# Optimization experiments

Measured on AMD Instinct MI355X. Metric: run time of the kernel, lower is better.

The kernel has to match this reference:

```python
import jax, jax.numpy as jnp
import numpy as np

N, HID, MAXD, B, NCLS, GRUH = 50000, 128, 16, 50, 10, 32


def setup_inputs() -> dict:
    key = jax.random.key(0)
    ks = jax.random.split(key, 18)
    s = 0.05
    nrm = lambda k, shp: (jax.random.normal(k, shp, jnp.float32) * s)
    return {
        "feature": jax.random.normal(ks[0], (N, HID), jnp.float32),
        "nbr_idx": jax.random.randint(ks[1], (N, MAXD), 0, N, dtype=jnp.int32),
        "deg": jax.random.randint(ks[2], (N,), 1, MAXD + 1, dtype=jnp.int32),
        "graph_ids": (jnp.arange(N, dtype=jnp.int32) * B) // N,
        # SAGEConv(lstm) params: LSTM(in=HID, hidden=HID) + fc_self/fc_neigh
        "lstm_Wih": nrm(ks[3], (4 * HID, HID)),
        "lstm_Whh": nrm(ks[4], (4 * HID, HID)),
        "lstm_bih": nrm(ks[5], (4 * HID,)),
        "lstm_bhh": nrm(ks[6], (4 * HID,)),
        "W_self": nrm(ks[7], (HID, HID)),
        "W_neigh": nrm(ks[8], (HID, HID)),
        "b_sage": nrm(ks[9], (HID,)),
        # GraphConv params
        "W_gc": nrm(ks[10], (HID, HID)),
        "b_gc": nrm(ks[11], (HID,)),
        # GRU params (h0=0 so weight_hh contributes nothing; only its bias matters)
        "Wih_gru": nrm(ks[12], (3 * GRUH, HID)),
        "bih_gru": nrm(ks[13], (3 * GRUH,)),
        "bhh_gru": nrm(ks[14], (3 * GRUH,)),
        # classifier (dropout is identity at eval)
        "W_cls": nrm(ks[15], (GRUH, NCLS)),
        "b_cls": nrm(ks[16], (NCLS,)),
    }


def _lstm_aggregate(feats, nbr_idx, deg, Wih, Whh, bih, bhh):
    # DGL SAGEConv 'lstm' reducer: run LSTM over each node's neighbor features,
    # take final hidden state. Implemented as a masked scan over padded lists.
    n, hdim = feats.shape
    h0 = jnp.zeros((n, hdim), feats.dtype)

    def step(carry, t):
        h, c = carry
        x = feats[jnp.take(nbr_idx, t, axis=1)]  # [N, HID] gather of t-th neighbor
        gates = x @ Wih.T + bih + h @ Whh.T + bhh
        i, f, g, o = jnp.split(gates, 4, axis=-1)  # torch gate order i,f,g,o
        c_new = jax.nn.sigmoid(f) * c + jax.nn.sigmoid(i) * jnp.tanh(g)
        h_new = jax.nn.sigmoid(o) * jnp.tanh(c_new)
        valid = (t < deg)[:, None]
        return (jnp.where(valid, h_new, h), jnp.where(valid, c_new, c)), None

    (hT, _), _ = jax.lax.scan(step, (h0, h0), jnp.arange(nbr_idx.shape[1]))
    return hT  # hidden at each node's last valid neighbor


def _graph_conv(h, nbr_idx, deg, W, b):
    # DGL GraphConv norm='both': D^-1/2 A D^-1/2 h W + b
    n, maxd = nbr_idx.shape
    norm = jax.lax.rsqrt(jnp.maximum(deg.astype(h.dtype), 1.0))
    hn = h * norm[:, None]
    mask = (jnp.arange(maxd, dtype=jnp.int32)[None, :] < deg[:, None]).astype(h.dtype)
    contrib = hn[nbr_idx.reshape(-1)] * mask.reshape(-1)[:, None]  # [N*MAXD, HID]
    dst = jnp.repeat(jnp.arange(n, dtype=jnp.int32), maxd)
    agg = jax.ops.segment_sum(contrib, dst, num_segments=n)
    return (agg * norm[:, None]) @ W + b


def _gru_step(x, Wih, bih, bhh):
    # single GRU step with h0 = 0 (seq_len == 1 in the original view(1, N, H))
    gh = x @ Wih.T + bih  # [N, 3*GRUH]
    xr, xz, xn = jnp.split(gh, 3, axis=-1)  # torch gate order r,z,n
    br, bz, bn = jnp.split(bhh, 3)
    r = jax.nn.sigmoid(xr + br)
    z = jax.nn.sigmoid(xz + bz)
    nst = jnp.tanh(xn + r * bn)
    return (1.0 - z) * nst  # h' = (1-z)*n + z*h0, h0 = 0


def reference(feature, nbr_idx, deg, graph_ids, lstm_Wih, lstm_Whh, lstm_bih,
              lstm_bhh, W_self, W_neigh, b_sage, W_gc, b_gc, Wih_gru, bih_gru,
              bhh_gru, W_cls, b_cls):
    # conv4: SAGEConv lstm -> relu
    h_nei = _lstm_aggregate(feature, nbr_idx, deg, lstm_Wih, lstm_Whh, lstm_bih, lstm_bhh)
    h = jax.nn.relu(feature @ W_self + h_nei @ W_neigh + b_sage)
    # conv2: GraphConv -> relu
    h = jax.nn.relu(_graph_conv(h, nbr_idx, deg, W_gc, b_gc))
    # GRU over seq_len=1, batch=N
    out = _gru_step(h, Wih_gru, bih_gru, bhh_gru)  # [N, 32]
    # dgl.mean_nodes: per-graph mean pool
    sums = jax.ops.segment_sum(out, graph_ids, num_segments=B)
    cnts = jax.ops.segment_sum(jnp.ones((out.shape[0],), out.dtype), graph_ids, num_segments=B)
    hg = sums / cnts[:, None]
    # classify (Dropout is identity in eval)
    return hg @ W_cls + b_cls  # [B, NCLS]
```

## Files before the change

kernel.cpp:

```cpp
#include <hip/hip_runtime.h>
#include <hip/hip_bf16.h>


#define NN     50000
#define HIDD   128
#define MAXD   16
#define NGRAPH 50
#define NCLSS  10
#define GRUH   32

typedef __attribute__((ext_vector_type(8))) short s16x8;
typedef __attribute__((ext_vector_type(4))) float f32x4;
typedef __hip_bfloat16 bf16;

#define MFMA16(a,b,c)  __builtin_amdgcn_mfma_f32_16x16x32_bf16((a),(b),(c),0,0,0)

__device__ __forceinline__ float bf2f(bf16 x) { return __bfloat162float(x); }
__device__ __forceinline__ bf16  f2bf(float x) { return __float2bfloat16(x); }
__device__ __forceinline__ s16x8 ldfrag(const bf16* p) { return *(const s16x8*)p; }

__device__ __forceinline__ float sigf(float x) {
  return __builtin_amdgcn_rcpf(1.0f + __expf(-x));
}
__device__ __forceinline__ float tanhf_(float x) {
  return 1.0f - 2.0f * __builtin_amdgcn_rcpf(1.0f + __expf(2.0f * x));
}

__device__ __forceinline__ void lgkm_barrier() {
  asm volatile("s_waitcnt lgkmcnt(0)\n\ts_barrier" ::: "memory");
}

__global__ void prep_kernel(const float* __restrict__ feat, const float* __restrict__ Wih,
                            const float* __restrict__ Whh, const float* __restrict__ bih,
                            const float* __restrict__ bhh, const float* __restrict__ Wself,
                            const float* __restrict__ Wneigh, const float* __restrict__ Wgc,
                            const float* __restrict__ Wgru,
                            bf16* featB, bf16* WihB, bf16* WhhB, bf16* WsT, bf16* WnT,
                            bf16* WgT, bf16* WgruB, float* biasS) {
  const int nf = NN * HIDD;
  const int total = nf + 2 * 65536 + 3 * 16384 + 12288 + 512;
  int stride = gridDim.x * blockDim.x;
  for (int idx = blockIdx.x * blockDim.x + threadIdx.x; idx < total; idx += stride) {
    if (idx < nf) { featB[idx] = f2bf(feat[idx]); continue; }
    int j = idx - nf;
    if (j < 65536) { WihB[j] = f2bf(Wih[j]); continue; }
    j -= 65536;
    if (j < 65536) { WhhB[j] = f2bf(Whh[j]); continue; }
    j -= 65536;
    if (j < 16384) { int c = j >> 7, k = j & 127; WsT[j] = f2bf(Wself[k * HIDD + c]); continue; }
    j -= 16384;
    if (j < 16384) { int c = j >> 7, k = j & 127; WnT[j] = f2bf(Wneigh[k * HIDD + c]); continue; }
    j -= 16384;
    if (j < 16384) { int c = j >> 7, k = j & 127; WgT[j] = f2bf(Wgc[k * HIDD + c]); continue; }
    j -= 16384;
    if (j < 12288) { WgruB[j] = f2bf(Wgru[j]); continue; }
    j -= 12288;
    biasS[j] = bih[j] + bhh[j];
  }
}

__global__ __launch_bounds__(256) void hist_kernel(const int* __restrict__ deg, int* hist) {
  __shared__ int lh[17];
  const int tid = threadIdx.x;
  if (tid < 17) lh[tid] = 0;
  __syncthreads();
  const int i = blockIdx.x * 256 + tid;
  if (i < NN) atomicAdd(&lh[deg[i]], 1);
  __syncthreads();
  if (tid < 17 && lh[tid]) atomicAdd(&hist[tid], lh[tid]);
}

__global__ __launch_bounds__(256) void scatter_kernel(const int* __restrict__ deg,
                                                      const int* __restrict__ hist,
                                                      int* __restrict__ resv,
                                                      int* __restrict__ perm) {
  __shared__ int lh[17], lbase[17], lpos[17];
  const int tid = threadIdx.x;
  if (tid < 17) { lh[tid] = 0; lpos[tid] = 0; }
  __syncthreads();
  const int i = blockIdx.x * 256 + tid;
  const int d = (i < NN) ? deg[i] : -1;
  if (d >= 0) atomicAdd(&lh[d], 1);
  __syncthreads();
  if (tid < 17) {
    int pre = 0;
    for (int k = tid + 1; k < 17; ++k) pre += hist[k];
    lbase[tid] = pre + (lh[tid] ? atomicAdd(&resv[tid], lh[tid]) : 0);
  }
  __syncthreads();
  if (d >= 0) {
    const int p = lbase[d] + atomicAdd(&lpos[d], 1);
    perm[p] = i;
  }
}

__global__ __launch_bounds__(512, 1) void lstm_kernel(const bf16* __restrict__ featB,
                                                      const bf16* __restrict__ WihB,
                                                      const bf16* __restrict__ WhhB,
                                                      const float* __restrict__ biasS,
                                                      const int* __restrict__ nbr_idx,
                                                      const int* __restrict__ deg,
                                                      const int* __restrict__ perm,
                                                      bf16* __restrict__ hTB) {
  __shared__ __align__(16) bf16 WiS[512 * 128];
  __shared__ __align__(16) bf16 Xs[2][32 * 136];
  __shared__ __align__(16) bf16 Hs[32 * 128];
  __shared__ int nbr_s[16 * 32];
  __shared__ int nodes_s[32];
  __shared__ int degs_s[32];

  const int tid = threadIdx.x;
  const int lane = tid & 63, w = tid >> 6;
  const int l15 = lane & 15, quad = lane >> 4;
  const int base = blockIdx.x * 32;
  const int colw = w * 16 + l15;

  if (tid < 32) {
    const int gi = base + tid;
    const int nd = (gi < NN) ? perm[gi] : -1;
    nodes_s[tid] = nd;
    degs_s[tid] = (nd >= 0) ? deg[nd] : 0;
  }
  __syncthreads();
  for (int e = tid; e < 16 * 32; e += 512) {
    const int row = e & 31, t = e >> 5;
    const int nd = nodes_s[row];
    nbr_s[t * 32 + row] = (nd >= 0) ? nbr_idx[nd * MAXD + t] : 0;
  }
  for (int e = tid; e < 32 * 64; e += 512) ((unsigned int*)Hs)[e] = 0u;
  {
    const int c = tid;
#pragma unroll
    for (int j = 0; j < 16; ++j)
      *(s16x8*)(WiS + c * 128 + ((j ^ (c & 15)) * 8)) = ldfrag(WihB + c * HIDD + j * 8);
  }

  s16x8 Bh[4][4];
#pragma unroll
  for (int q = 0; q < 4; ++q)
#pragma unroll
    for (int kt = 0; kt < 4; ++kt) {
      Bh[q][kt] = ldfrag(WhhB + (q * 128 + colw) * HIDD + kt * 32 + quad * 8);
      asm volatile("" : "+v"(Bh[q][kt]));
    }
  float biasv[4];
#pragma unroll
  for (int q = 0; q < 4; ++q) biasv[q] = biasS[q * 128 + colw];

  __syncthreads();
  const int maxdeg = degs_s[0];

  int mydeg[2][4];
#pragma unroll
  for (int rt = 0; rt < 2; ++rt)
#pragma unroll
    for (int rr = 0; rr < 4; ++rr) mydeg[rt][rr] = degs_s[rt * 16 + quad * 4 + rr];

  const int srow = tid >> 4, schk = tid & 15;
  {
    const int nb0 = nbr_s[0 * 32 + srow];
    *(s16x8*)(&Xs[0][srow * 136 + schk * 8]) = ldfrag(featB + (size_t)nb0 * HIDD + schk * 8);
  }
  float cst[2][4] = {{0.f, 0.f, 0.f, 0.f}, {0.f, 0.f, 0.f, 0.f}};
  lgkm_barrier();

  for (int t = 0; t < maxdeg; ++t) {
    s16x8 xstage;
    const bool do_stage = (t + 1 < maxdeg);
    if (do_stage) {
      const int nb1 = nbr_s[(t + 1) * 32 + srow];
      xstage = ldfrag(featB + (size_t)nb1 * HIDD + schk * 8);
    }

    f32x4 acc[2][4];
#pragma unroll
    for (int rt = 0; rt < 2; ++rt)
#pragma unroll
      for (int q = 0; q < 4; ++q) acc[rt][q] = (f32x4){0.f, 0.f, 0.f, 0.f};

    const bf16* Xc = &Xs[t & 1][0];
#pragma unroll
    for (int kt = 0; kt < 4; ++kt) {
      s16x8 ax0 = ldfrag(Xc + (0 * 16 + l15) * 136 + (kt * 4 + quad) * 8);
      s16x8 ax1 = ldfrag(Xc + (1 * 16 + l15) * 136 + (kt * 4 + quad) * 8);
#pragma unroll
      for (int q = 0; q < 4; ++q) {
        const int col = q * 128 + colw;
        const s16x8 bi = ldfrag(WiS + col * 128 + (((kt * 4 + quad) ^ (col & 15)) * 8));
        acc[0][q] = MFMA16(ax0, bi, acc[0][q]);
        acc[1][q] = MFMA16(ax1, bi, acc[1][q]);
      }
    }

    if (t > 0) {
#pragma unroll
      for (int rt = 0; rt < 2; ++rt)
#pragma unroll
        for (int kt = 0; kt < 4; ++kt) {
          const int m = rt * 16 + l15;
          const int k = kt * 32 + quad * 8;
          const s16x8 ah = ldfrag(Hs + m * 128 + (k ^ (l15 * 8)));
#pragma unroll
          for (int q = 0; q < 4; ++q)
            acc[rt][q] = MFMA16(ah, Bh[q][kt], acc[rt][q]);
        }
    }
    lgkm_barrier();

    if (do_stage)
      *(s16x8*)(&Xs[(t + 1) & 1][srow * 136 + schk * 8]) = xstage;

#pragma unroll
    for (int rt = 0; rt < 2; ++rt)
#pragma unroll
      for (int rr = 0; rr < 4; ++rr) {
        const int row = rt * 16 + quad * 4 + rr;
        const float g_i = acc[rt][0][rr] + biasv[0];
        const float g_f = acc[rt][1][rr] + biasv[1];
        const float g_g = acc[rt][2][rr] + biasv[2];
        const float g_o = acc[rt][3][rr] + biasv[3];
        const float iv = sigf(g_i), fv = sigf(g_f);
        const float gv = tanhf_(g_g), ov = sigf(g_o);
        const float cn = fv * cst[rt][rr] + iv * gv;
        const float hn = ov * tanhf_(cn);
        if (t < mydeg[rt][rr]) {
          cst[rt][rr] = cn;
          Hs[row * 128 + (colw ^ ((row & 15) * 8))] = f2bf(hn);
        }
      }
    lgkm_barrier();
  }

  for (int e = tid; e < 32 * 16; e += 512) {
    const int row = e >> 4, j = e & 15;
    const int nd = nodes_s[row];
    if (nd >= 0) {
      const s16x8 v = ldfrag(Hs + row * 128 + ((j * 8) ^ ((row & 15) * 8)));
      *(s16x8*)(hTB + (size_t)nd * HIDD + j * 8) = v;
    }
  }
}

__global__ __launch_bounds__(256) void sage_kernel(const bf16* __restrict__ featB,
                                                   const bf16* __restrict__ hTB,
                                                   const bf16* __restrict__ WsT,
                                                   const bf16* __restrict__ WnT,
                                                   const float* __restrict__ b_sage,
                                                   const int* __restrict__ deg,
                                                   bf16* __restrict__ h1n) {
  const int lane = threadIdx.x & 63, wave = threadIdx.x >> 6;
  const int l15 = lane & 15, quad = lane >> 4;
  const int nb = blockIdx.x * 64 + wave * 16;
  int arow = nb + l15; if (arow >= NN) arow = NN - 1;
  s16x8 Fa[4], Ha[4];
#pragma unroll
  for (int kt = 0; kt < 4; ++kt) {
    Fa[kt] = ldfrag(featB + (size_t)arow * HIDD + kt * 32 + quad * 8);
    Ha[kt] = ldfrag(hTB + (size_t)arow * HIDD + kt * 32 + quad * 8);
  }
  int nodes[4]; float nrm[4];
#pragma unroll
  for (int r = 0; r < 4; ++r) {
    const int nd = nb + quad * 4 + r;
    nodes[r] = nd;
    nrm[r] = rsqrtf((float)deg[(nd < NN) ? nd : (NN - 1)]);
  }
  for (int ct = 0; ct < 8; ++ct) {
    const int col = ct * 16 + l15;
    f32x4 acc = {0.f, 0.f, 0.f, 0.f};
#pragma unroll
    for (int kt = 0; kt < 4; ++kt) {
      acc = MFMA16(Fa[kt], ldfrag(WsT + col * HIDD + kt * 32 + quad * 8), acc);
      acc = MFMA16(Ha[kt], ldfrag(WnT + col * HIDD + kt * 32 + quad * 8), acc);
    }
    const float bb = b_sage[col];
#pragma unroll
    for (int r = 0; r < 4; ++r)
      if (nodes[r] < NN) {
        const float v = fmaxf(acc[r] + bb, 0.f) * nrm[r];
        h1n[(size_t)nodes[r] * HIDD + col] = f2bf(v);
      }
  }
}

__global__ __launch_bounds__(256) void agg_kernel(const bf16* __restrict__ h1n,
                                                  const int* __restrict__ nbr_idx,
                                                  const int* __restrict__ deg,
                                                  bf16* __restrict__ aggB) {
  const int wave = threadIdx.x >> 6, lane = threadIdx.x & 63;
  const int node = blockIdx.x * 4 + wave;
  if (node >= NN) return;
  const int d = deg[node];
  const int idx_l = nbr_idx[node * MAXD + (lane & 15)];
  const int c = lane * 2;
  float a0 = 0.f, a1 = 0.f;
  for (int t = 0; t < d; ++t) {
    const int nbr = __shfl(idx_l, t, 64);
    const __hip_bfloat162 v = *(const __hip_bfloat162*)(h1n + (size_t)nbr * HIDD + c);
    a0 += __bfloat162float(v.x);
    a1 += __bfloat162float(v.y);
  }
  const float nm = rsqrtf((float)d);
  aggB[(size_t)node * HIDD + c]     = f2bf(a0 * nm);
  aggB[(size_t)node * HIDD + c + 1] = f2bf(a1 * nm);
}

__global__ __launch_bounds__(256) void gc_gemm_kernel(const bf16* __restrict__ aggB,
                                                      const bf16* __restrict__ WgT,
                                                      const float* __restrict__ b_gc,
                                                      bf16* __restrict__ h2B) {
  const int lane = threadIdx.x & 63, wave = threadIdx.x >> 6;
  const int l15 = lane & 15, quad = lane >> 4;
  const int nb = blockIdx.x * 64 + wave * 16;
  int arow = nb + l15; if (arow >= NN) arow = NN - 1;
  s16x8 A[4];
#pragma unroll
  for (int kt = 0; kt < 4; ++kt) A[kt] = ldfrag(aggB + (size_t)arow * HIDD + kt * 32 + quad * 8);
  for (int ct = 0; ct < 8; ++ct) {
    const int col = ct * 16 + l15;
    f32x4 acc = {0.f, 0.f, 0.f, 0.f};
#pragma unroll
    for (int kt = 0; kt < 4; ++kt)
      acc = MFMA16(A[kt], ldfrag(WgT + col * HIDD + kt * 32 + quad * 8), acc);
    const float bb = b_gc[col];
#pragma unroll
    for (int r = 0; r < 4; ++r) {
      const int node = nb + quad * 4 + r;
      if (node < NN) h2B[(size_t)node * HIDD + col] = f2bf(fmaxf(acc[r] + bb, 0.f));
    }
  }
}

__global__ __launch_bounds__(256) void gru_kernel(const bf16* __restrict__ h2B,
                                                  const bf16* __restrict__ WgruB,
                                                  const float* __restrict__ bih,
                                                  const float* __restrict__ bhh,
                                                  float* __restrict__ gout) {
  const int lane = threadIdx.x & 63, wave = threadIdx.x >> 6;
  const int l15 = lane & 15, quad = lane >> 4;
  const int nb = blockIdx.x * 64 + wave * 16;
  int arow = nb + l15; if (arow >= NN) arow = NN - 1;
  s16x8 A[4];
#pragma unroll
  for (int kt = 0; kt < 4; ++kt) A[kt] = ldfrag(h2B + (size_t)arow * HIDD + kt * 32 + quad * 8);
  f32x4 acc[6];
#pragma unroll
  for (int ct = 0; ct < 6; ++ct) {
    f32x4 a = {0.f, 0.f, 0.f, 0.f};
#pragma unroll
    for (int kt = 0; kt < 4; ++kt)
      a = MFMA16(A[kt], ldfrag(WgruB + (ct * 16 + l15) * HIDD + kt * 32 + quad * 8), a);
    acc[ct] = a;
  }
#pragma unroll
  for (int u = 0; u < 2; ++u) {
    const int cu = 16 * u + l15;
    const float br = bih[cu] + bhh[cu];
    const float bz = bih[32 + cu] + bhh[32 + cu];
    const float bni = bih[64 + cu];
    const float bnh = bhh[64 + cu];
#pragma unroll
    for (int r = 0; r < 4; ++r) {
      const int node = nb + quad * 4 + r;
      if (node < NN) {
        const float rv = sigf(acc[u][r] + br);
        const float zv = sigf(acc[2 + u][r] + bz);
        const float nv = tanhf_(acc[4 + u][r] + bni + rv * bnh);
        gout[(size_t)node * GRUH + cu] = (1.f - zv) * nv;
      }
    }
  }
}

#define POOL_CHUNK 512
__global__ __launch_bounds__(256) void pool_partial_kernel(const float* __restrict__ gout,
                                                           const int* __restrict__ gids,
                                                           float* __restrict__ sums,
                                                           float* __restrict__ cnts) {
  __shared__ float ls[NGRAPH * GRUH];
  __shared__ float lc[NGRAPH];
  const int tid = threadIdx.x;
  for (int i = tid; i < NGRAPH * GRUH; i += 256) ls[i] = 0.f;
  if (tid < NGRAPH) lc[tid] = 0.f;
  __syncthreads();

  const int wave = tid >> 6, lane = tid & 63;
  const int c = lane & 31, half = lane >> 5;
  const int base = blockIdx.x * POOL_CHUNK + wave * (POOL_CHUNK / 8);

  float accv = 0.f, ccnt = 0.f;
  int curg = -1;
  for (int it = 0; it < POOL_CHUNK / 16; ++it) {
    const int n = base + it * 2 + half;
    if (n < NN) {
      const int g = gids[n];
      const float v = gout[(size_t)n * GRUH + c];
      if (g != curg) {
        if (curg >= 0) {
          atomicAdd(&ls[curg * GRUH + c], accv);
          if (c == 0) atomicAdd(&lc[curg], ccnt);
        }
        curg = g; accv = 0.f; ccnt = 0.f;
      }
      accv += v; ccnt += 1.f;
    }
  }
  if (curg >= 0) {
    atomicAdd(&ls[curg * GRUH + c], accv);
    if (c == 0) atomicAdd(&lc[curg], ccnt);
  }
  __syncthreads();
  for (int i = tid; i < NGRAPH * GRUH; i += 256)
    if (ls[i] != 0.f) atomicAdd(&sums[i], ls[i]);
  if (tid < NGRAPH && lc[tid] != 0.f) atomicAdd(&cnts[tid], lc[tid]);
}

__global__ __launch_bounds__(256) void pool_final_kernel(const float* __restrict__ sums,
                                                         const float* __restrict__ cnts,
                                                         const float* __restrict__ Wcls,
                                                         const float* __restrict__ bcls,
                                                         float* __restrict__ out) {
  const int idx = blockIdx.x * blockDim.x + threadIdx.x;
  if (idx >= NGRAPH * NCLSS) return;
  const int g = idx / NCLSS, k = idx % NCLSS;
  const float inv = 1.0f / cnts[g];
  float acc = bcls[k];
#pragma unroll
  for (int cc = 0; cc < GRUH; ++cc)
    acc += sums[g * GRUH + cc] * inv * Wcls[cc * NCLSS + k];
  out[idx] = acc;
}

extern "C" void kernel_launch(void* const* d_in, const int* in_sizes, int n_in,
                              void* d_out, int out_size, void* d_ws, size_t ws_size,
                              hipStream_t stream) {
  const float* feature  = (const float*)d_in[0];
  const int*   nbr_idx  = (const int*)d_in[1];
  const int*   deg      = (const int*)d_in[2];
  const int*   gids     = (const int*)d_in[3];
  const float* lstm_Wih = (const float*)d_in[4];
  const float* lstm_Whh = (const float*)d_in[5];
  const float* lstm_bih = (const float*)d_in[6];
  const float* lstm_bhh = (const float*)d_in[7];
  const float* W_self   = (const float*)d_in[8];
  const float* W_neigh  = (const float*)d_in[9];
  const float* b_sage   = (const float*)d_in[10];
  const float* W_gc     = (const float*)d_in[11];
  const float* b_gc     = (const float*)d_in[12];
  const float* Wih_gru  = (const float*)d_in[13];
  const float* bih_gru  = (const float*)d_in[14];
  const float* bhh_gru  = (const float*)d_in[15];
  const float* W_cls    = (const float*)d_in[16];
  const float* b_cls    = (const float*)d_in[17];

  char* ws = (char*)d_ws;
  bf16*  featB = (bf16*)(ws + 0);
  bf16*  hTB   = (bf16*)(ws + 12800000);
  bf16*  h1nB  = (bf16*)(ws + 25600000);
  bf16*  aggB  = (bf16*)(ws + 38400000);
  bf16*  h2B   = (bf16*)(ws + 51200000);
  float* gout  = (float*)(ws + 12800000);
  const size_t wo = 64000000;
  bf16*  WihB  = (bf16*)(ws + wo);
  bf16*  WhhB  = (bf16*)(ws + wo + 131072);
  bf16*  WsT   = (bf16*)(ws + wo + 262144);
  bf16*  WnT   = (bf16*)(ws + wo + 294912);
  bf16*  WgT   = (bf16*)(ws + wo + 327680);
  bf16*  WgruB = (bf16*)(ws + wo + 360448);
  float* biasS = (float*)(ws + wo + 385024);
  int*   perm  = (int*)(ws + 65000000);
  int*   hist  = (int*)(ws + 65400000);
  int*   resv  = hist + 17;
  float* psums = (float*)(ws + 65401216);
  float* pcnts = psums + NGRAPH * GRUH;

  prep_kernel<<<3072, 256, 0, stream>>>(feature, lstm_Wih, lstm_Whh, lstm_bih, lstm_bhh,
                                        W_self, W_neigh, W_gc, Wih_gru,
                                        featB, WihB, WhhB, WsT, WnT, WgT, WgruB, biasS);
  hipMemsetAsync(hist, 0, 34 * sizeof(int), stream);
  hipMemsetAsync(psums, 0, (NGRAPH * GRUH + NGRAPH) * sizeof(float), stream);
  hist_kernel<<<196, 256, 0, stream>>>(deg, hist);
  scatter_kernel<<<196, 256, 0, stream>>>(deg, hist, resv, perm);
  lstm_kernel<<<1563, 512, 0, stream>>>(featB, WihB, WhhB, biasS, nbr_idx, deg, perm, hTB);
  sage_kernel<<<782, 256, 0, stream>>>(featB, hTB, WsT, WnT, b_sage, deg, h1nB);
  agg_kernel<<<12500, 256, 0, stream>>>(h1nB, nbr_idx, deg, aggB);
  gc_gemm_kernel<<<782, 256, 0, stream>>>(aggB, WgT, b_gc, h2B);
  gru_kernel<<<782, 256, 0, stream>>>(h2B, WgruB, bih_gru, bhh_gru, gout);
  pool_partial_kernel<<<(NN + POOL_CHUNK - 1) / POOL_CHUNK, 256, 0, stream>>>(gout, gids, psums, pcnts);
  pool_final_kernel<<<2, 256, 0, stream>>>(psums, pcnts, W_cls, b_cls, (float*)d_out);
}
```

Before: 447.9 us.

## Double-buffer LSTM hidden state to drop a barrier; fuse GraphConv GEMM with GRU

```diff
diff --git a/kernel.cpp b/kernel.cpp
--- a/kernel.cpp
+++ b/kernel.cpp
@@ -102,9 +102,10 @@
                                                       const int* __restrict__ deg,
                                                       const int* __restrict__ perm,
                                                       bf16* __restrict__ hTB) {
-  __shared__ __align__(16) bf16 WiS[512 * 128];
-  __shared__ __align__(16) bf16 Xs[2][32 * 136];
-  __shared__ __align__(16) bf16 Hs[32 * 128];
+  __shared__ __align__(16) bf16 WiA[512 * 64];
+  __shared__ __align__(16) bf16 WiB[384 * 64];
+  __shared__ __align__(16) bf16 Xs[2][32 * 128];
+  __shared__ __align__(16) bf16 Hs[2][32 * 128];
   __shared__ int nbr_s[16 * 32];
   __shared__ int nodes_s[32];
   __shared__ int degs_s[32];
@@ -114,6 +115,7 @@
   const int l15 = lane & 15, quad = lane >> 4;
   const int base = blockIdx.x * 32;
   const int colw = w * 16 + l15;
+  const int srow = tid >> 4, schk = tid & 15;
 
   if (tid < 32) {
     const int gi = base + tid;
@@ -127,15 +129,19 @@
     const int nd = nodes_s[row];
     nbr_s[t * 32 + row] = (nd >= 0) ? nbr_idx[nd * MAXD + t] : 0;
   }
-  for (int e = tid; e < 32 * 64; e += 512) ((unsigned int*)Hs)[e] = 0u;
   {
     const int c = tid;
 #pragma unroll
-    for (int j = 0; j < 16; ++j)
-      *(s16x8*)(WiS + c * 128 + ((j ^ (c & 15)) * 8)) = ldfrag(WihB + c * HIDD + j * 8);
-  }
-
-  s16x8 Bh[4][4];
+    for (int j = 0; j < 8; ++j)
+      *(s16x8*)(WiA + c * 64 + ((j ^ (c & 7)) * 8)) = ldfrag(WihB + c * HIDD + j * 8);
+    if (c < 384) {
+#pragma unroll
+      for (int j = 0; j < 8; ++j)
+        *(s16x8*)(WiB + c * 64 + ((j ^ (c & 7)) * 8)) = ldfrag(WihB + c * HIDD + 64 + j * 8);
+    }
+  }
+
+  s16x8 Bh[4][4], BiR[2];
 #pragma unroll
   for (int q = 0; q < 4; ++q)
 #pragma unroll
@@ -143,6 +149,11 @@
       Bh[q][kt] = ldfrag(WhhB + (q * 128 + colw) * HIDD + kt * 32 + quad * 8);
       asm volatile("" : "+v"(Bh[q][kt]));
     }
+#pragma unroll
+  for (int kt = 2; kt < 4; ++kt) {
+    BiR[kt - 2] = ldfrag(WihB + (3 * 128 + colw) * HIDD + kt * 32 + quad * 8);
+    asm volatile("" : "+v"(BiR[kt - 2]));
+  }
   float biasv[4];
 #pragma unroll
   for (int q = 0; q < 4; ++q) biasv[q] = biasS[q * 128 + colw];
@@ -156,15 +167,17 @@
 #pragma unroll
     for (int rr = 0; rr < 4; ++rr) mydeg[rt][rr] = degs_s[rt * 16 + quad * 4 + rr];
 
-  const int srow = tid >> 4, schk = tid & 15;
   {
     const int nb0 = nbr_s[0 * 32 + srow];
-    *(s16x8*)(&Xs[0][srow * 136 + schk * 8]) = ldfrag(featB + (size_t)nb0 * HIDD + schk * 8);
+    *(s16x8*)(Xs[0] + srow * 128 + ((schk ^ (srow & 15)) * 8)) =
+        ldfrag(featB + (size_t)nb0 * HIDD + schk * 8);
   }
   float cst[2][4] = {{0.f, 0.f, 0.f, 0.f}, {0.f, 0.f, 0.f, 0.f}};
+  float hprev[2][4] = {{0.f, 0.f, 0.f, 0.f}, {0.f, 0.f, 0.f, 0.f}};
   lgkm_barrier();
 
   for (int t = 0; t < maxdeg; ++t) {
+    const int cur = t & 1, nxt = cur ^ 1;
     s16x8 xstage;
     const bool do_stage = (t + 1 < maxdeg);
     if (do_stage) {
@@ -178,15 +191,19 @@
 #pragma unroll
       for (int q = 0; q < 4; ++q) acc[rt][q] = (f32x4){0.f, 0.f, 0.f, 0.f};
 
-    const bf16* Xc = &Xs[t & 1][0];
 #pragma unroll
     for (int kt = 0; kt < 4; ++kt) {
-      s16x8 ax0 = ldfrag(Xc + (0 * 16 + l15) * 136 + (kt * 4 + quad) * 8);
-      s16x8 ax1 = ldfrag(Xc + (1 * 16 + l15) * 136 + (kt * 4 + quad) * 8);
+      const int oct = kt * 4 + quad;
+      const int o8 = (kt & 1) * 4 + quad;
+      const s16x8 ax0 = ldfrag(Xs[cur] + (0 * 16 + l15) * 128 + ((oct ^ l15) * 8));
+      const s16x8 ax1 = ldfrag(Xs[cur] + (1 * 16 + l15) * 128 + ((oct ^ l15) * 8));
 #pragma unroll
       for (int q = 0; q < 4; ++q) {
         const int col = q * 128 + colw;
-        const s16x8 bi = ldfrag(WiS + col * 128 + (((kt * 4 + quad) ^ (col & 15)) * 8));
+        s16x8 bi;
+        if (kt < 2)      bi = ldfrag(WiA + col * 64 + ((o8 ^ (col & 7)) * 8));
+        else if (q < 3)  bi = ldfrag(WiB + col * 64 + ((o8 ^ (col & 7)) * 8));
+        else             bi = BiR[kt - 2];
         acc[0][q] = MFMA16(ax0, bi, acc[0][q]);
         acc[1][q] = MFMA16(ax1, bi, acc[1][q]);
       }
@@ -198,17 +215,13 @@
 #pragma unroll
         for (int kt = 0; kt < 4; ++kt) {
           const int m = rt * 16 + l15;
-          const int k = kt * 32 + quad * 8;
-          const s16x8 ah = ldfrag(Hs + m * 128 + (k ^ (l15 * 8)));
+          const int oct = kt * 4 + quad;
+          const s16x8 ah = ldfrag(Hs[cur] + m * 128 + ((oct ^ l15) * 8));
 #pragma unroll
           for (int q = 0; q < 4; ++q)
             acc[rt][q] = MFMA16(ah, Bh[q][kt], acc[rt][q]);
         }
     }
-    lgkm_barrier();
-
-    if (do_stage)
-      *(s16x8*)(&Xs[(t + 1) & 1][srow * 136 + schk * 8]) = xstage;
 
 #pragma unroll
     for (int rt = 0; rt < 2; ++rt)
@@ -222,20 +235,25 @@
         const float iv = sigf(g_i), fv = sigf(g_f);
         const float gv = tanhf_(g_g), ov = sigf(g_o);
         const float cn = fv * cst[rt][rr] + iv * gv;
-        const float hn = ov * tanhf_(cn);
-        if (t < mydeg[rt][rr]) {
-          cst[rt][rr] = cn;
-          Hs[row * 128 + (colw ^ ((row & 15) * 8))] = f2bf(hn);
-        }
+        const float hn_new = ov * tanhf_(cn);
+        const bool act = (t < mydeg[rt][rr]);
+        if (act) cst[rt][rr] = cn;
+        const float hn = act ? hn_new : hprev[rt][rr];
+        hprev[rt][rr] = hn;
+        Hs[nxt][row * 128 + (((colw >> 3) ^ (row & 15)) * 8) + (colw & 7)] = f2bf(hn);
       }
+    if (do_stage)
+      *(s16x8*)(Xs[nxt] + srow * 128 + ((schk ^ (srow & 15)) * 8)) = xstage;
+
     lgkm_barrier();
   }
 
+  const bf16* Hf = Hs[maxdeg & 1];
   for (int e = tid; e < 32 * 16; e += 512) {
     const int row = e >> 4, j = e & 15;
     const int nd = nodes_s[row];
     if (nd >= 0) {
-      const s16x8 v = ldfrag(Hs + row * 128 + ((j * 8) ^ ((row & 15) * 8)));
+      const s16x8 v = ldfrag(Hf + row * 128 + ((j ^ (row & 15)) * 8));
       *(s16x8*)(hTB + (size_t)nd * HIDD + j * 8) = v;
     }
   }
@@ -305,10 +323,14 @@
   aggB[(size_t)node * HIDD + c + 1] = f2bf(a1 * nm);
 }
 
-__global__ __launch_bounds__(256) void gc_gemm_kernel(const bf16* __restrict__ aggB,
-                                                      const bf16* __restrict__ WgT,
-                                                      const float* __restrict__ b_gc,
-                                                      bf16* __restrict__ h2B) {
+__global__ __launch_bounds__(256) void gcgru_kernel(const bf16* __restrict__ aggB,
+                                                    const bf16* __restrict__ WgT,
+                                                    const float* __restrict__ b_gc,
+                                                    const bf16* __restrict__ WgruB,
+                                                    const float* __restrict__ bih,
+                                                    const float* __restrict__ bhh,
+                                                    float* __restrict__ gout) {
+  __shared__ __align__(16) bf16 H2[64 * 136];
   const int lane = threadIdx.x & 63, wave = threadIdx.x >> 6;
   const int l15 = lane & 15, quad = lane >> 4;
   const int nb = blockIdx.x * 64 + wave * 16;
@@ -324,32 +346,21 @@
       acc = MFMA16(A[kt], ldfrag(WgT + col * HIDD + kt * 32 + quad * 8), acc);
     const float bb = b_gc[col];
 #pragma unroll
-    for (int r = 0; r < 4; ++r) {
-      const int node = nb + quad * 4 + r;
-      if (node < NN) h2B[(size_t)node * HIDD + col] = f2bf(fmaxf(acc[r] + bb, 0.f));
-    }
-  }
-}
-
-__global__ __launch_bounds__(256) void gru_kernel(const bf16* __restrict__ h2B,
-                                                  const bf16* __restrict__ WgruB,
-                                                  const float* __restrict__ bih,
-                                                  const float* __restrict__ bhh,
-                                                  float* __restrict__ gout) {
-  const int lane = threadIdx.x & 63, wave = threadIdx.x >> 6;
-  const int l15 = lane & 15, quad = lane >> 4;
-  const int nb = blockIdx.x * 64 + wave * 16;
-  int arow = nb + l15; if (arow >= NN) arow = NN - 1;
-  s16x8 A[4];
-#pragma unroll
-  for (int kt = 0; kt < 4; ++kt) A[kt] = ldfrag(h2B + (size_t)arow * HIDD + kt * 32 + quad * 8);
+    for (int r = 0; r < 4; ++r)
+      H2[(wave * 16 + quad * 4 + r) * 136 + col] = f2bf(fmaxf(acc[r] + bb, 0.f));
+  }
+  __syncthreads();
+  s16x8 A2[4];
+#pragma unroll
+  for (int kt = 0; kt < 4; ++kt)
+    A2[kt] = ldfrag(H2 + (wave * 16 + l15) * 136 + kt * 32 + quad * 8);
   f32x4 acc[6];
 #pragma unroll
   for (int ct = 0; ct < 6; ++ct) {
     f32x4 a = {0.f, 0.f, 0.f, 0.f};
 #pragma unroll
     for (int kt = 0; kt < 4; ++kt)
-      a = MFMA16(A[kt], ldfrag(WgruB + (ct * 16 + l15) * HIDD + kt * 32 + quad * 8), a);
+      a = MFMA16(A2[kt], ldfrag(WgruB + (ct * 16 + l15) * HIDD + kt * 32 + quad * 8), a);
     acc[ct] = a;
   }
 #pragma unroll
@@ -458,7 +469,6 @@
   bf16*  hTB   = (bf16*)(ws + 12800000);
   bf16*  h1nB  = (bf16*)(ws + 25600000);
   bf16*  aggB  = (bf16*)(ws + 38400000);
-  bf16*  h2B   = (bf16*)(ws + 51200000);
   float* gout  = (float*)(ws + 12800000);
   const size_t wo = 64000000;
   bf16*  WihB  = (bf16*)(ws + wo);
@@ -484,8 +494,7 @@
   lstm_kernel<<<1563, 512, 0, stream>>>(featB, WihB, WhhB, biasS, nbr_idx, deg, perm, hTB);
   sage_kernel<<<782, 256, 0, stream>>>(featB, hTB, WsT, WnT, b_sage, deg, h1nB);
   agg_kernel<<<12500, 256, 0, stream>>>(h1nB, nbr_idx, deg, aggB);
-  gc_gemm_kernel<<<782, 256, 0, stream>>>(aggB, WgT, b_gc, h2B);
-  gru_kernel<<<782, 256, 0, stream>>>(h2B, WgruB, bih_gru, bhh_gru, gout);
+  gcgru_kernel<<<782, 256, 0, stream>>>(aggB, WgT, b_gc, WgruB, bih_gru, bhh_gru, gout);
   pool_partial_kernel<<<(NN + POOL_CHUNK - 1) / POOL_CHUNK, 256, 0, stream>>>(gout, gids, psums, pcnts);
   pool_final_kernel<<<2, 256, 0, stream>>>(psums, pcnts, W_cls, b_cls, (float*)d_out);
 }
```

Measured after the change: 429.7 us. -4.1%, faster.
